# Performance work log

Measured on AMD Instinct MI355X. Metric: run time of the kernel, lower is better.

## Reference

```python
import jax, jax.numpy as jnp
import numpy as np

B, S, D, H = 4, 1024, 1024, 16
HD = D // H  # head_dim = 64
NEG = -1e9  # stands in for float('-inf') in masked_fill; numerically safe


def setup_inputs() -> dict:
    key = jax.random.key(0)
    ks = jax.random.split(key, 8)
    q = jax.random.normal(ks[0], (B, S, D), dtype=jnp.float32)
    k = jax.random.normal(ks[1], (B, S, D), dtype=jnp.float32)
    v = jax.random.normal(ks[2], (B, S, D), dtype=jnp.float32)
    # padding mask: True marks padded positions; pad out the tail of each sequence
    pos = jnp.arange(S)
    lengths = jnp.array([S, S - 64, S - 128, S - 256])
    padding_mask = pos[None, :] >= lengths[:, None]  # [B, S] bool
    # additive causal mask: 0 on/below diagonal, NEG above
    causal_mask = jnp.where(jnp.tril(jnp.ones((S, S), dtype=bool)), 0.0, NEG).astype(jnp.float32)
    scale = 1.0 / np.sqrt(D)
    Wq = jax.random.normal(ks[3], (D, D), dtype=jnp.float32) * scale
    Wk = jax.random.normal(ks[4], (D, D), dtype=jnp.float32) * scale
    Wv = jax.random.normal(ks[5], (D, D), dtype=jnp.float32) * scale
    Wo = jax.random.normal(ks[6], (D, D), dtype=jnp.float32) * scale
    return {"q": q, "k": k, "v": v, "padding_mask": padding_mask,
            "causal_mask": causal_mask, "Wq": Wq, "Wk": Wk, "Wv": Wv,
            "Wo": Wo, "n_heads": H}


def reference(q, k, v, padding_mask, causal_mask, Wq, Wk, Wv, Wo, n_heads):
    b, s, d = q.shape
    hd = d // n_heads
    # projections (nn.Linear: x @ W^T, no bias)
    qp = (q @ Wq.T).reshape(b, s, n_heads, hd).transpose(0, 2, 1, 3)  # [b,h,s,hd]
    kp = (k @ Wk.T).reshape(b, s, n_heads, hd).transpose(0, 2, 1, 3)
    vp = (v @ Wv.T).reshape(b, s, n_heads, hd).transpose(0, 2, 1, 3)
    scores = jnp.einsum('bhqd,bhkd->bhqk', qp, kp) / jnp.sqrt(jnp.float32(hd))
    # masked_fill(padding_mask, -inf): mask broadcast over heads and query dim
    scores = jnp.where(padding_mask[:, None, None, :], NEG, scores)
    scores = scores + causal_mask  # additive causal mask
    attn = jax.nn.softmax(scores, axis=-1)
    out = jnp.einsum('bhqk,bhkd->bhqd', attn, vp)
    out = out.transpose(0, 2, 1, 3).reshape(b, s, d)
    return out @ Wo.T
```

## Files before the change

### kernel.cpp

```cpp
#include <hip/hip_runtime.h>
#include <hip/hip_bf16.h>

#define BB 4
#define SS 1024
#define DD 1024
#define HH 16
#define HD 64
#define MM (BB*SS)


typedef __bf16 bf16x8 __attribute__((ext_vector_type(8)));
typedef __bf16 bf16x4 __attribute__((ext_vector_type(4)));
typedef float  f32x4  __attribute__((ext_vector_type(4)));

__global__ __launch_bounds__(256) void expand_mask(const void* __restrict__ pmraw,
                                                   float* __restrict__ madd,
                                                   int n)
{
    const unsigned char* bytes = (const unsigned char*)pmraw;
    __shared__ int isbool;
    if (threadIdx.x == 0) isbool = 0;
    __syncthreads();
    int flag = 0;
    for (int idx = threadIdx.x; idx < n; idx += 256) {
        if ((idx & 3) && bytes[idx]) flag = 1;
    }
    if (flag) atomicOr(&isbool, 1);
    __syncthreads();
    int i = blockIdx.x * 256 + threadIdx.x;
    if (i < n) {
        int v = isbool ? (int)bytes[i] : ((const int*)pmraw)[i];
        madd[i] = (v != 0) ? -1e9f : 0.0f;
    }
}

__global__ __launch_bounds__(256) void conv3(const float* __restrict__ s0,
                                             const float* __restrict__ s1,
                                             const float* __restrict__ s2,
                                             __bf16* __restrict__ d0,
                                             __bf16* __restrict__ d1,
                                             __bf16* __restrict__ d2)
{
    const float* s; __bf16* d;
    if (blockIdx.y == 0)      { s = s0; d = d0; }
    else if (blockIdx.y == 1) { s = s1; d = d1; }
    else                      { s = s2; d = d2; }
    int i = (blockIdx.x * 256 + threadIdx.x) * 4;
    float4 x = *(const float4*)(s + i);
    bf16x4 o;
    o[0] = (__bf16)x.x; o[1] = (__bf16)x.y;
    o[2] = (__bf16)x.z; o[3] = (__bf16)x.w;
    *(bf16x4*)(d + i) = o;
}

__global__ __launch_bounds__(256) void conv4(const float* __restrict__ s0,
                                             const float* __restrict__ s1,
                                             const float* __restrict__ s2,
                                             const float* __restrict__ s3,
                                             __bf16* __restrict__ d0,
                                             __bf16* __restrict__ d1,
                                             __bf16* __restrict__ d2,
                                             __bf16* __restrict__ d3)
{
    const float* s; __bf16* d;
    if (blockIdx.y == 0)      { s = s0; d = d0; }
    else if (blockIdx.y == 1) { s = s1; d = d1; }
    else if (blockIdx.y == 2) { s = s2; d = d2; }
    else                      { s = s3; d = d3; }
    int i = (blockIdx.x * 256 + threadIdx.x) * 4;
    float4 x = *(const float4*)(s + i);
    bf16x4 o;
    o[0] = (__bf16)x.x; o[1] = (__bf16)x.y;
    o[2] = (__bf16)x.z; o[3] = (__bf16)x.w;
    *(bf16x4*)(d + i) = o;
}

#define GM 128
#define GN 64
#define GK 64

__global__ __launch_bounds__(256) void gemm_qkv(const __bf16* __restrict__ qb,
                                                const __bf16* __restrict__ kb,
                                                const __bf16* __restrict__ vb,
                                                const __bf16* __restrict__ Wqb,
                                                const __bf16* __restrict__ Wkb,
                                                const __bf16* __restrict__ Wvb,
                                                __bf16* __restrict__ Qp,
                                                __bf16* __restrict__ Kp,
                                                __bf16* __restrict__ VpT)
{
    __shared__ __align__(16) __bf16 As[GM][GK];
    __shared__ __align__(16) __bf16 Bs[GN][GK];

    const __bf16 *A, *W; __bf16* C;
    const int z = blockIdx.z;
    if (z == 0)      { A = qb; W = Wqb; C = Qp;  }
    else if (z == 1) { A = kb; W = Wkb; C = Kp;  }
    else             { A = vb; W = Wvb; C = VpT; }

    const int tid  = threadIdx.x;
    const int lane = tid & 63;
    const int w    = tid >> 6;
    const int l15  = lane & 15;
    const int quad = lane >> 4;
    const int wr   = w >> 1;
    const int wc   = w & 1;

    const int m0 = blockIdx.y * GM;
    const int n0 = blockIdx.x * GN;

    const int srow = tid >> 3;
    const int scol = (tid & 7) * 8;

    const __bf16* gA = A + (size_t)(m0 + srow) * DD + scol;
    const __bf16* gB = W + (size_t)(n0 + srow) * DD + scol;

    f32x4 acc[4][2] = {};

    for (int k0 = 0; k0 < DD; k0 += GK) {
        __syncthreads();
        #pragma unroll
        for (int c = 0; c < 4; ++c)
            __builtin_amdgcn_global_load_lds(
                (const __attribute__((address_space(1))) void*)(gA + (size_t)c * 32 * DD + k0),
                (__attribute__((address_space(3))) void*)(&As[c * 32 + srow][scol]), 16, 0, 0);
        #pragma unroll
        for (int c = 0; c < 2; ++c)
            __builtin_amdgcn_global_load_lds(
                (const __attribute__((address_space(1))) void*)(gB + (size_t)c * 32 * DD + k0),
                (__attribute__((address_space(3))) void*)(&Bs[c * 32 + srow][scol]), 16, 0, 0);
        __syncthreads();

        #pragma unroll
        for (int ks = 0; ks < 2; ++ks) {
            bf16x8 af[4], bf[2];
            #pragma unroll
            for (int mt = 0; mt < 4; ++mt)
                af[mt] = *(const bf16x8*)&As[wr * 64 + mt * 16 + l15][ks * 32 + quad * 8];
            #pragma unroll
            for (int nt = 0; nt < 2; ++nt)
                bf[nt] = *(const bf16x8*)&Bs[wc * 32 + nt * 16 + l15][ks * 32 + quad * 8];
            #pragma unroll
            for (int mt = 0; mt < 4; ++mt)
                #pragma unroll
                for (int nt = 0; nt < 2; ++nt)
                    acc[mt][nt] = __builtin_amdgcn_mfma_f32_16x16x32_bf16(
                        af[mt], bf[nt], acc[mt][nt], 0, 0, 0);
        }
    }

    if (z == 0) {
        #pragma unroll
        for (int mt = 0; mt < 4; ++mt)
            #pragma unroll
            for (int nt = 0; nt < 2; ++nt)
                #pragma unroll
                for (int r = 0; r < 4; ++r)
                    acc[mt][nt][r] *= 0.125f;
    }

    if (z == 2) {
        #pragma unroll
        for (int mt = 0; mt < 4; ++mt)
            #pragma unroll
            for (int nt = 0; nt < 2; ++nt) {
                bf16x4 o;
                #pragma unroll
                for (int r = 0; r < 4; ++r) o[r] = (__bf16)acc[mt][nt][r];
                const int n = n0 + wc * 32 + nt * 16 + l15;
                const int m = m0 + wr * 64 + mt * 16 + quad * 4;
                *(bf16x4*)&C[(size_t)n * MM + m] = o;
            }
    } else {
        #pragma unroll
        for (int mt = 0; mt < 4; ++mt)
            #pragma unroll
            for (int nt = 0; nt < 2; ++nt)
                #pragma unroll
                for (int r = 0; r < 4; ++r)
                    C[(size_t)(m0 + wr * 64 + mt * 16 + quad * 4 + r) * DD +
                      (n0 + wc * 32 + nt * 16 + l15)] = (__bf16)acc[mt][nt][r];
    }
}

__global__ __launch_bounds__(256) void gemm_wo(const __bf16* __restrict__ A,
                                               const __bf16* __restrict__ W,
                                               float* __restrict__ C)
{
    __shared__ __align__(16) __bf16 As[64][64];
    __shared__ __align__(16) __bf16 Bs[64][64];

    const int tid  = threadIdx.x;
    const int lane = tid & 63;
    const int w    = tid >> 6;
    const int l15  = lane & 15;
    const int quad = lane >> 4;
    const int wr   = w >> 1;
    const int wc   = w & 1;

    const int m0 = blockIdx.y * 64;
    const int n0 = blockIdx.x * 64;

    const int srow = tid >> 3;
    const int scol = (tid & 7) * 8;

    const __bf16* gA = A + (size_t)(m0 + srow) * DD + scol;
    const __bf16* gB = W + (size_t)(n0 + srow) * DD + scol;

    f32x4 acc[2][2] = {};

    for (int k0 = 0; k0 < DD; k0 += 64) {
        __syncthreads();
        #pragma unroll
        for (int c = 0; c < 2; ++c)
            __builtin_amdgcn_global_load_lds(
                (const __attribute__((address_space(1))) void*)(gA + (size_t)c * 32 * DD + k0),
                (__attribute__((address_space(3))) void*)(&As[c * 32 + srow][scol]), 16, 0, 0);
        #pragma unroll
        for (int c = 0; c < 2; ++c)
            __builtin_amdgcn_global_load_lds(
                (const __attribute__((address_space(1))) void*)(gB + (size_t)c * 32 * DD + k0),
                (__attribute__((address_space(3))) void*)(&Bs[c * 32 + srow][scol]), 16, 0, 0);
        __syncthreads();

        #pragma unroll
        for (int ks = 0; ks < 2; ++ks) {
            bf16x8 af[2], bf[2];
            #pragma unroll
            for (int mt = 0; mt < 2; ++mt)
                af[mt] = *(const bf16x8*)&As[wr * 32 + mt * 16 + l15][ks * 32 + quad * 8];
            #pragma unroll
            for (int nt = 0; nt < 2; ++nt)
                bf[nt] = *(const bf16x8*)&Bs[wc * 32 + nt * 16 + l15][ks * 32 + quad * 8];
            #pragma unroll
            for (int mt = 0; mt < 2; ++mt)
                #pragma unroll
                for (int nt = 0; nt < 2; ++nt)
                    acc[mt][nt] = __builtin_amdgcn_mfma_f32_16x16x32_bf16(
                        af[mt], bf[nt], acc[mt][nt], 0, 0, 0);
        }
    }

    #pragma unroll
    for (int mt = 0; mt < 2; ++mt)
        #pragma unroll
        for (int nt = 0; nt < 2; ++nt)
            #pragma unroll
            for (int r = 0; r < 4; ++r)
                C[(size_t)(m0 + wr * 32 + mt * 16 + quad * 4 + r) * DD +
                  (n0 + wc * 32 + nt * 16 + l15)] = acc[mt][nt][r];
}

#define PSTR 72
#define OSTR 68

__global__ __launch_bounds__(256, 2) void flash_attn(const __bf16* __restrict__ Qp,
                                                     const __bf16* __restrict__ Kp,
                                                     const __bf16* __restrict__ VpT,
                                                     const float* __restrict__ maskadd,
                                                     __bf16* __restrict__ Op)
{
    __shared__ __align__(16) unsigned char smem[4 * 64 * PSTR * 2];
    __bf16 (*Pl)[64][PSTR]  = (__bf16 (*)[64][PSTR])smem;
    float  (*Obuf)[64][OSTR] = (float (*)[64][OSTR])smem;

    const int tid  = threadIdx.x;
    const int lane = tid & 63;
    const int w    = tid >> 6;
    const int l15  = lane & 15;
    const int quad = lane >> 4;
    const int h    = w & 1;
    const int tile = w >> 1;

    const int bh = blockIdx.x;
    const int hh = bh & (HH - 1);
    const int b  = bh >> 4;
    const int p  = blockIdx.y;
    const int m  = tile ? (15 - p) : p;

    const size_t hbase = (size_t)b * SS * DD + (size_t)hh * HD;
    const int q0 = m * 64;

    bf16x8 qf[4][2];
    #pragma unroll
    for (int qt = 0; qt < 4; ++qt) {
        const __bf16* qp = Qp + hbase + (size_t)(q0 + qt * 16 + l15) * DD + quad * 8;
        qf[qt][0] = *(const bf16x8*)qp;
        qf[qt][1] = *(const bf16x8*)(qp + 32);
    }

    const __bf16* vt = VpT + (size_t)(hh * HD) * MM + b * SS;
    const float* madd = maskadd + b * SS;

    f32x4 Ov[4][4] = {};
    float lsumq[4] = {};

    for (int kt = h; kt <= m; kt += 2) {
        const int kbase = kt * 64;
        const bool diag = (kt == m);

        f32x4 St[4][4];
        #pragma unroll
        for (int kg = 0; kg < 4; ++kg) {
            const __bf16* kp = Kp + hbase + (size_t)(kbase + kg * 16 + l15) * DD + quad * 8;
            bf16x8 kf0 = *(const bf16x8*)kp;
            bf16x8 kf1 = *(const bf16x8*)(kp + 32);
            #pragma unroll
            for (int qt = 0; qt < 4; ++qt) {
                f32x4 s = {};
                s = __builtin_amdgcn_mfma_f32_16x16x32_bf16(kf0, qf[qt][0], s, 0, 0, 0);
                s = __builtin_amdgcn_mfma_f32_16x16x32_bf16(kf1, qf[qt][1], s, 0, 0, 0);
                St[kg][qt] = s;
            }
        }

        #pragma unroll
        for (int kg = 0; kg < 4; ++kg) {
            const float4 mr = *(const float4*)&madd[kbase + kg * 16 + quad * 4];
            #pragma unroll
            for (int qt = 0; qt < 4; ++qt) {
                const int i = q0 + qt * 16 + l15;
                bf16x4 pk;
                #pragma unroll
                for (int r = 0; r < 4; ++r) {
                    const int j = kbase + kg * 16 + quad * 4 + r;
                    float pv = __expf(St[kg][qt][r] + ((const float*)&mr)[r]);
                    if (diag && j > i) pv = 0.f;
                    lsumq[qt] += pv;
                    pk[r] = (__bf16)pv;
                }
                *(bf16x4*)&Pl[w][qt * 16 + l15][kg * 16 + quad * 4] = pk;
            }
        }

        bf16x8 pf[4][2];
        #pragma unroll
        for (int qt = 0; qt < 4; ++qt) {
            pf[qt][0] = *(const bf16x8*)&Pl[w][qt * 16 + l15][quad * 8];
            pf[qt][1] = *(const bf16x8*)&Pl[w][qt * 16 + l15][quad * 8 + 32];
        }

        #pragma unroll
        for (int dt = 0; dt < 4; ++dt) {
            const __bf16* vp = vt + (size_t)(dt * 16 + l15) * MM + kbase + quad * 8;
            bf16x8 vf0 = *(const bf16x8*)vp;
            bf16x8 vf1 = *(const bf16x8*)(vp + 32);
            #pragma unroll
            for (int qt = 0; qt < 4; ++qt) {
                Ov[qt][dt] = __builtin_amdgcn_mfma_f32_16x16x32_bf16(pf[qt][0], vf0, Ov[qt][dt], 0, 0, 0);
                Ov[qt][dt] = __builtin_amdgcn_mfma_f32_16x16x32_bf16(pf[qt][1], vf1, Ov[qt][dt], 0, 0, 0);
            }
        }
    }

    #pragma unroll
    for (int off = 16; off < 64; off <<= 1)
        #pragma unroll
        for (int qt = 0; qt < 4; ++qt)
            lsumq[qt] += __shfl_xor(lsumq[qt], off);

    __syncthreads();
    if (h == 1) {
        #pragma unroll
        for (int qt = 0; qt < 4; ++qt) {
            #pragma unroll
            for (int dt = 0; dt < 4; ++dt)
                #pragma unroll
                for (int r = 0; r < 4; ++r)
                    Obuf[tile][qt * 16 + quad * 4 + r][dt * 16 + l15] = Ov[qt][dt][r];
            if (quad == 0)
                Obuf[tile][qt * 16 + l15][64] = lsumq[qt];
        }
    }
    __syncthreads();
    if (h == 0) {
        #pragma unroll
        for (int qt = 0; qt < 4; ++qt) {
            const float rcp = 1.0f / (lsumq[qt] + Obuf[tile][qt * 16 + l15][64]);
            float rq[4];
            #pragma unroll
            for (int r = 0; r < 4; ++r) rq[r] = __shfl(rcp, quad * 4 + r);
            #pragma unroll
            for (int dt = 0; dt < 4; ++dt)
                #pragma unroll
                for (int r = 0; r < 4; ++r) {
                    const int i = q0 + qt * 16 + quad * 4 + r;
                    float o = Ov[qt][dt][r] +
                              Obuf[tile][qt * 16 + quad * 4 + r][dt * 16 + l15];
                    Op[hbase + (size_t)i * DD + dt * 16 + l15] = (__bf16)(o * rq[r]);
                }
        }
    }
}

extern "C" void kernel_launch(void* const* d_in, const int* in_sizes, int n_in,
                              void* d_out, int out_size, void* d_ws, size_t ws_size,
                              hipStream_t stream)
{
    const float* q  = (const float*)d_in[0];
    const float* k  = (const float*)d_in[1];
    const float* v  = (const float*)d_in[2];
    const void*  pm = d_in[3];
    const float* Wq = (const float*)d_in[5];
    const float* Wk = (const float*)d_in[6];
    const float* Wv = (const float*)d_in[7];
    const float* Wo = (const float*)d_in[8];

    char* ws = (char*)d_ws;
    float* madd = (float*)ws;
    const size_t MB = 1024 * 1024;
    char* base = ws + 65536;

    __bf16* qb  = (__bf16*)(base +  0 * MB);
    __bf16* kb  = (__bf16*)(base +  8 * MB);
    __bf16* vb  = (__bf16*)(base + 16 * MB);
    __bf16* Wqb = (__bf16*)(base + 24 * MB);
    __bf16* Wkb = (__bf16*)(base + 26 * MB);
    __bf16* Wvb = (__bf16*)(base + 28 * MB);
    __bf16* Wob = (__bf16*)(base + 30 * MB);
    __bf16* Qp  = (__bf16*)(base + 32 * MB);
    __bf16* Kp  = (__bf16*)(base + 40 * MB);
    __bf16* VpT = (__bf16*)(base + 48 * MB);
    __bf16* Op  = qb;

    float* out = (float*)d_out;
    const int NT = MM * DD;
    const int NW = DD * DD;

    expand_mask<<<(BB * SS) / 256, 256, 0, stream>>>(pm, madd, BB * SS);
    conv3<<<dim3(NT / 1024, 3), 256, 0, stream>>>(q, k, v, qb, kb, vb);
    conv4<<<dim3(NW / 1024, 4), 256, 0, stream>>>(Wq, Wk, Wv, Wo, Wqb, Wkb, Wvb, Wob);

    dim3 gg(DD / GN, MM / GM, 3);
    gemm_qkv<<<gg, 256, 0, stream>>>(qb, kb, vb, Wqb, Wkb, Wvb, Qp, Kp, VpT);

    dim3 ga(BB * HH, 8);
    flash_attn<<<ga, 256, 0, stream>>>(Qp, Kp, VpT, madd, Op);

    dim3 gw(DD / 64, MM / 64);
    gemm_wo<<<gw, 256, 0, stream>>>(Op, Wob, out);
}
```

Measured before the change: 230.2 us.

## Merge conversion kernels, enlarge Wo GEMM tile, and swap grid order for weight reuse

The separate activation and weight fp32-to-bf16 conversion kernels become one launch, with the fourth grid row covering all four weight matrices. The output-projection GEMM moves from 64x64 to 128x64 tiles with four M-subtiles per wave, raising MFMA work per LDS load. Both GEMMs now put M on grid x and N on grid y, so consecutive blocks share the same weight tile and may reuse it in L2. The trade-off is fewer blocks for the Wo GEMM (512 instead of 1024) and more accumulator registers.

```diff
diff --git a/kernel.cpp b/kernel.cpp
--- a/kernel.cpp
+++ b/kernel.cpp
@@ -34,40 +34,36 @@
     }
 }
 
-__global__ __launch_bounds__(256) void conv3(const float* __restrict__ s0,
-                                             const float* __restrict__ s1,
-                                             const float* __restrict__ s2,
-                                             __bf16* __restrict__ d0,
-                                             __bf16* __restrict__ d1,
-                                             __bf16* __restrict__ d2)
-{
-    const float* s; __bf16* d;
-    if (blockIdx.y == 0)      { s = s0; d = d0; }
-    else if (blockIdx.y == 1) { s = s1; d = d1; }
-    else                      { s = s2; d = d2; }
-    int i = (blockIdx.x * 256 + threadIdx.x) * 4;
-    float4 x = *(const float4*)(s + i);
-    bf16x4 o;
-    o[0] = (__bf16)x.x; o[1] = (__bf16)x.y;
-    o[2] = (__bf16)x.z; o[3] = (__bf16)x.w;
-    *(bf16x4*)(d + i) = o;
-}
-
-__global__ __launch_bounds__(256) void conv4(const float* __restrict__ s0,
-                                             const float* __restrict__ s1,
-                                             const float* __restrict__ s2,
-                                             const float* __restrict__ s3,
-                                             __bf16* __restrict__ d0,
-                                             __bf16* __restrict__ d1,
-                                             __bf16* __restrict__ d2,
-                                             __bf16* __restrict__ d3)
-{
-    const float* s; __bf16* d;
-    if (blockIdx.y == 0)      { s = s0; d = d0; }
-    else if (blockIdx.y == 1) { s = s1; d = d1; }
-    else if (blockIdx.y == 2) { s = s2; d = d2; }
-    else                      { s = s3; d = d3; }
-    int i = (blockIdx.x * 256 + threadIdx.x) * 4;
+__global__ __launch_bounds__(256) void convall(const float* __restrict__ q,
+                                               const float* __restrict__ k,
+                                               const float* __restrict__ v,
+                                               const float* __restrict__ Wq,
+                                               const float* __restrict__ Wk,
+                                               const float* __restrict__ Wv,
+                                               const float* __restrict__ Wo,
+                                               __bf16* __restrict__ qb,
+                                               __bf16* __restrict__ kb,
+                                               __bf16* __restrict__ vb,
+                                               __bf16* __restrict__ Wqb,
+                                               __bf16* __restrict__ Wkb,
+                                               __bf16* __restrict__ Wvb,
+                                               __bf16* __restrict__ Wob)
+{
+    const float* s; __bf16* d; int i;
+    if (blockIdx.y < 3) {
+        if (blockIdx.y == 0)      { s = q; d = qb; }
+        else if (blockIdx.y == 1) { s = k; d = kb; }
+        else                      { s = v; d = vb; }
+        i = (blockIdx.x * 256 + threadIdx.x) * 4;
+    } else {
+        const int wsel = blockIdx.x >> 10;
+        const int lx   = blockIdx.x & 1023;
+        if (wsel == 0)      { s = Wq; d = Wqb; }
+        else if (wsel == 1) { s = Wk; d = Wkb; }
+        else if (wsel == 2) { s = Wv; d = Wvb; }
+        else                { s = Wo; d = Wob; }
+        i = (lx * 256 + threadIdx.x) * 4;
+    }
     float4 x = *(const float4*)(s + i);
     bf16x4 o;
     o[0] = (__bf16)x.x; o[1] = (__bf16)x.y;
@@ -106,8 +102,8 @@
     const int wr   = w >> 1;
     const int wc   = w & 1;
 
-    const int m0 = blockIdx.y * GM;
-    const int n0 = blockIdx.x * GN;
+    const int m0 = blockIdx.x * GM;
+    const int n0 = blockIdx.y * GN;
 
     const int srow = tid >> 3;
     const int scol = (tid & 7) * 8;
@@ -187,8 +183,8 @@
                                                const __bf16* __restrict__ W,
                                                float* __restrict__ C)
 {
-    __shared__ __align__(16) __bf16 As[64][64];
-    __shared__ __align__(16) __bf16 Bs[64][64];
+    __shared__ __align__(16) __bf16 As[GM][GK];
+    __shared__ __align__(16) __bf16 Bs[GN][GK];
 
     const int tid  = threadIdx.x;
     const int lane = tid & 63;
@@ -198,8 +194,8 @@
     const int wr   = w >> 1;
     const int wc   = w & 1;
 
-    const int m0 = blockIdx.y * 64;
-    const int n0 = blockIdx.x * 64;
+    const int m0 = blockIdx.x * GM;
+    const int n0 = blockIdx.y * GN;
 
     const int srow = tid >> 3;
     const int scol = (tid & 7) * 8;
@@ -207,12 +203,12 @@
     const __bf16* gA = A + (size_t)(m0 + srow) * DD + scol;
     const __bf16* gB = W + (size_t)(n0 + srow) * DD + scol;
 
-    f32x4 acc[2][2] = {};
-
-    for (int k0 = 0; k0 < DD; k0 += 64) {
+    f32x4 acc[4][2] = {};
+
+    for (int k0 = 0; k0 < DD; k0 += GK) {
         __syncthreads();
         #pragma unroll
-        for (int c = 0; c < 2; ++c)
+        for (int c = 0; c < 4; ++c)
             __builtin_amdgcn_global_load_lds(
                 (const __attribute__((address_space(1))) void*)(gA + (size_t)c * 32 * DD + k0),
                 (__attribute__((address_space(3))) void*)(&As[c * 32 + srow][scol]), 16, 0, 0);
@@ -225,15 +221,15 @@
 
         #pragma unroll
         for (int ks = 0; ks < 2; ++ks) {
-            bf16x8 af[2], bf[2];
-            #pragma unroll
-            for (int mt = 0; mt < 2; ++mt)
-                af[mt] = *(const bf16x8*)&As[wr * 32 + mt * 16 + l15][ks * 32 + quad * 8];
+            bf16x8 af[4], bf[2];
+            #pragma unroll
+            for (int mt = 0; mt < 4; ++mt)
+                af[mt] = *(const bf16x8*)&As[wr * 64 + mt * 16 + l15][ks * 32 + quad * 8];
             #pragma unroll
             for (int nt = 0; nt < 2; ++nt)
                 bf[nt] = *(const bf16x8*)&Bs[wc * 32 + nt * 16 + l15][ks * 32 + quad * 8];
             #pragma unroll
-            for (int mt = 0; mt < 2; ++mt)
+            for (int mt = 0; mt < 4; ++mt)
                 #pragma unroll
                 for (int nt = 0; nt < 2; ++nt)
                     acc[mt][nt] = __builtin_amdgcn_mfma_f32_16x16x32_bf16(
@@ -242,12 +238,12 @@
     }
 
     #pragma unroll
-    for (int mt = 0; mt < 2; ++mt)
+    for (int mt = 0; mt < 4; ++mt)
         #pragma unroll
         for (int nt = 0; nt < 2; ++nt)
             #pragma unroll
             for (int r = 0; r < 4; ++r)
-                C[(size_t)(m0 + wr * 32 + mt * 16 + quad * 4 + r) * DD +
+                C[(size_t)(m0 + wr * 64 + mt * 16 + quad * 4 + r) * DD +
                   (n0 + wc * 32 + nt * 16 + l15)] = acc[mt][nt][r];
 }
 
@@ -425,18 +421,17 @@
 
     float* out = (float*)d_out;
     const int NT = MM * DD;
-    const int NW = DD * DD;
 
     expand_mask<<<(BB * SS) / 256, 256, 0, stream>>>(pm, madd, BB * SS);
-    conv3<<<dim3(NT / 1024, 3), 256, 0, stream>>>(q, k, v, qb, kb, vb);
-    conv4<<<dim3(NW / 1024, 4), 256, 0, stream>>>(Wq, Wk, Wv, Wo, Wqb, Wkb, Wvb, Wob);
-
-    dim3 gg(DD / GN, MM / GM, 3);
+    convall<<<dim3(NT / 1024, 4), 256, 0, stream>>>(q, k, v, Wq, Wk, Wv, Wo,
+                                                    qb, kb, vb, Wqb, Wkb, Wvb, Wob);
+
+    dim3 gg(MM / GM, DD / GN, 3);
     gemm_qkv<<<gg, 256, 0, stream>>>(qb, kb, vb, Wqb, Wkb, Wvb, Qp, Kp, VpT);
 
     dim3 ga(BB * HH, 8);
     flash_attn<<<ga, 256, 0, stream>>>(Qp, Kp, VpT, madd, Op);
 
-    dim3 gw(DD / 64, MM / 64);
+    dim3 gw(MM / GM, DD / GN);
     gemm_wo<<<gw, 256, 0, stream>>>(Op, Wob, out);
 }
```

New measurement: 226.3 us. Within noise of the previous version (-1.7%).
